# Performance work log

Hardware: AMD Instinct MI355X
Metric: run time of the kernel (lower is better)

## Reference

```python
import jax, jax.numpy as jnp
import numpy as np
from jax.ops import segment_sum

N = 100000
E = 3200000
IN_DIM = 256
OUT_DIM = 64
LN_EPS = 1e-5
NEG_SLOPE = 0.01


def setup_inputs() -> dict:
    key = jax.random.key(0)
    k1, k2, k3, k4, k5 = jax.random.split(key, 5)
    x = jax.random.normal(k1, (N, IN_DIM), dtype=jnp.float32)
    edge_index = jax.random.randint(k2, (2, E), 0, N, dtype=jnp.int32)
    edge_weight = jax.random.uniform(k3, (E,), dtype=jnp.float32)
    # GCNConv params (glorot-ish scale) + LayerNorm params
    W = jax.random.normal(k4, (IN_DIM, OUT_DIM), dtype=jnp.float32) / np.sqrt(IN_DIM)
    b = jnp.zeros((OUT_DIM,), dtype=jnp.float32)
    gamma = jnp.ones((OUT_DIM,), dtype=jnp.float32)
    beta = jnp.zeros((OUT_DIM,), dtype=jnp.float32)
    return {"x": x, "edge_index": edge_index, "edge_weight": edge_weight,
            "W": W, "b": b, "gamma": gamma, "beta": beta}


def _gcn_forward(x, edge_index, edge_weight, W, b, gamma, beta):
    n = x.shape[0]
    # add self-loops with weight 1 (PyG GCNConv default)
    loops = jnp.arange(n, dtype=edge_index.dtype)
    src = jnp.concatenate([edge_index[0], loops])   # [E+N] message sources
    dst = jnp.concatenate([edge_index[1], loops])   # [E+N] aggregation targets
    ew = jnp.concatenate([edge_weight, jnp.ones((n,), dtype=edge_weight.dtype)])
    # symmetric normalization: deg computed on dst via weighted scatter
    deg = segment_sum(ew, dst, num_segments=n)                   # [N]
    dinv = jnp.where(deg > 0, jax.lax.rsqrt(deg), 0.0)           # deg^{-1/2}
    norm = dinv[src] * ew * dinv[dst]                            # [E+N]
    h = x @ W                                                    # [N, OUT]
    agg = segment_sum(h[src] * norm[:, None], dst, num_segments=n)  # [N, OUT]
    y = agg + b
    # leaky_relu then LayerNorm over last dim
    y = jnp.where(y >= 0, y, NEG_SLOPE * y)
    mu = jnp.mean(y, axis=-1, keepdims=True)
    var = jnp.mean(jnp.square(y - mu), axis=-1, keepdims=True)
    return (y - mu) * jax.lax.rsqrt(var + LN_EPS) * gamma + beta


def reference(x, edge_index, edge_weight, W, b, gamma, beta):
    return _gcn_forward(x, edge_index, edge_weight, W, b, gamma, beta)
```

## Files before the change

### kernel.cpp

```cpp
#include <hip/hip_runtime.h>

#define NN 100000
#define NE 3200000
#define OVCAP 65536

#define BINSZ 64
#define NBIN ((NN + BINSZ - 1) / BINSZ)
#define MAXPB 4096
#define SCAT_BLOCKS 512

struct OvEnt { int dst; int src; float ew; int pad; };


__global__ void k_zero(int* __restrict__ bincnt, int* __restrict__ ovcnt, int n) {
    int i = blockIdx.x * 256 + threadIdx.x;
    if (i < n) bincnt[i] = 0;
    if (i == 0) *ovcnt = 0;
}

__global__ __launch_bounds__(256) void k_binscatter(
    const int* __restrict__ src, const int* __restrict__ dst,
    const float* __restrict__ ew, int* __restrict__ bincnt,
    uint2* __restrict__ binbuf, int cap,
    OvEnt* __restrict__ ov, int* __restrict__ ovcnt, int e) {
    __shared__ int hist[NBIN];
    int t = threadIdx.x;
    int chunk = (e + gridDim.x - 1) / gridDim.x;
    int beg = blockIdx.x * chunk;
    int end = beg + chunk; if (end > e) end = e;
    for (int j = t; j < NBIN; j += 256) hist[j] = 0;
    __syncthreads();
    for (int i = beg + t; i < end; i += 256)
        atomicAdd(&hist[dst[i] >> 6], 1);
    __syncthreads();
    for (int j = t; j < NBIN; j += 256) {
        int c = hist[j];
        hist[j] = (c > 0) ? atomicAdd(&bincnt[j], c) : 0;
    }
    __syncthreads();
    for (int i = beg + t; i < end; i += 256) {
        int s = src[i], d = dst[i];
        float w = ew[i];
        int bin = d >> 6;
        int pos = atomicAdd(&hist[bin], 1);
        if (pos < cap) {
            unsigned key = (unsigned)s | ((unsigned)(d & 63) << 17);
            binbuf[(size_t)bin * cap + pos] = make_uint2(key, __float_as_uint(w));
        } else {
            int op = atomicAdd(ovcnt, 1);
            if (op < OVCAP) { OvEnt t2; t2.dst = d; t2.src = s; t2.ew = w; t2.pad = 0; ov[op] = t2; }
        }
    }
}

__global__ __launch_bounds__(256) void k_deg2(
    const int* __restrict__ bincnt, const uint2* __restrict__ binbuf, int cap,
    const OvEnt* __restrict__ ov, const int* __restrict__ ovcnt,
    float* __restrict__ dinv, int n) {
    __shared__ float sdeg[BINSZ];
    int bin = blockIdx.x, t = threadIdx.x;
    if (t < BINSZ) sdeg[t] = 0.f;
    __syncthreads();
    int cnt = bincnt[bin];
    int bc = cnt < cap ? cnt : cap;
    const uint2* base = binbuf + (size_t)bin * cap;
    for (int i = t; i < bc; i += 256) {
        uint2 v = base[i];
        atomicAdd(&sdeg[(v.x >> 17) & 63u], __uint_as_float(v.y));
    }
    if (cnt > cap) {
        int on = *ovcnt; if (on > OVCAP) on = OVCAP;
        for (int j = t; j < on; j += 256) {
            OvEnt e2 = ov[j];
            if ((e2.dst >> 6) == bin) atomicAdd(&sdeg[e2.dst & 63], e2.ew);
        }
    }
    __syncthreads();
    if (t < BINSZ) {
        int g = bin * BINSZ + t;
        if (g < n) dinv[g] = rsqrtf(1.0f + sdeg[t]);
    }
}

__global__ __launch_bounds__(512) void k_sortgather(
    const float* __restrict__ h, const float* __restrict__ dinv,
    const int* __restrict__ bincnt, const uint2* __restrict__ binbuf, int cap,
    const OvEnt* __restrict__ ov, const int* __restrict__ ovcnt,
    const float* __restrict__ bias, const float* __restrict__ gamma,
    const float* __restrict__ beta, float* __restrict__ out, int n) {
    __shared__ uint2 sbuf[MAXPB];
    __shared__ float sd[BINSZ];
    __shared__ int hcnt[BINSZ];
    __shared__ int hoff[BINSZ];
    __shared__ int noff[BINSZ];
    int bin = blockIdx.x, t = threadIdx.x;
    int lane = t & 63, wid = t >> 6;

    if (t < BINSZ) {
        hcnt[t] = 0;
        int g = bin * BINSZ + t;
        sd[t] = (g < n) ? dinv[g] : 0.f;
    }
    __syncthreads();
    int cnt = bincnt[bin];
    int bc = cnt < cap ? cnt : cap;
    const uint2* base = binbuf + (size_t)bin * cap;

    uint2 ent[8];
    int ne = 0;
#pragma unroll
    for (int p = 0; p < 8; p++) {
        int idx = t + p * 512;
        if (idx < bc) { ent[p] = base[idx]; ne = p + 1; }
    }
#pragma unroll
    for (int p = 0; p < 8; p++)
        if (p < ne) atomicAdd(&hcnt[(int)((ent[p].x >> 17) & 63u)], 1);
    __syncthreads();
    if (t < 64) {
        int v = hcnt[t], inc = v;
#pragma unroll
        for (int o2 = 1; o2 < 64; o2 <<= 1) {
            int u = __shfl_up(inc, o2, 64);
            if (t >= o2) inc += u;
        }
        int excl = inc - v;
        hoff[t] = excl;
        noff[t] = excl;
    }
    __syncthreads();
#pragma unroll
    for (int p = 0; p < 8; p++) {
        if (p < ne) {
            int dl = (int)((ent[p].x >> 17) & 63u);
            int pos = atomicAdd(&hoff[dl], 1);
            sbuf[pos] = ent[p];
        }
    }
    __syncthreads();

    int sov = (cnt > cap);
    float bi = bias[lane], ga = gamma[lane], be = beta[lane];
    for (int dl = wid; dl < BINSZ; dl += 8) {
        int g = bin * BINSZ + dl;
        if (g >= n) break;
        float di = sd[dl];
        float acc = h[(size_t)g * 64 + lane] * di * di;
        int start = noff[dl], c0 = hcnt[dl];
        for (int j = 0; j < c0; j += 64) {
            int c = c0 - j; if (c > 64) c = 64;
            int s = 0; float w = 0.f;
            if (lane < c) {
                uint2 v = sbuf[start + j + lane];
                s = (int)(v.x & 0x1FFFFu);
                w = __uint_as_float(v.y) * dinv[s] * di;
            }
            int i2 = 0;
            for (; i2 + 16 <= c; i2 += 16) {
                float hv[16], wv[16];
#pragma unroll
                for (int q = 0; q < 16; q++) {
                    int si = __shfl(s, i2 + q, 64);
                    wv[q] = __shfl(w, i2 + q, 64);
                    hv[q] = h[(size_t)si * 64 + lane];
                }
#pragma unroll
                for (int q = 0; q < 16; q++) acc += hv[q] * wv[q];
            }
            if (i2 < c) {
                float hv[16], wv[16];
                int rem = c - i2;
#pragma unroll
                for (int q = 0; q < 16; q++) {
                    if (q < rem) {
                        int si = __shfl(s, i2 + q, 64);
                        wv[q] = __shfl(w, i2 + q, 64);
                        hv[q] = h[(size_t)si * 64 + lane];
                    } else { wv[q] = 0.f; hv[q] = 0.f; }
                }
#pragma unroll
                for (int q = 0; q < 16; q++) acc += hv[q] * wv[q];
            }
        }
        if (sov) {
            int on = *ovcnt; if (on > OVCAP) on = OVCAP;
            for (int j2 = 0; j2 < on; j2++) {
                OvEnt e2 = ov[j2];
                if (e2.dst == g)
                    acc += h[(size_t)e2.src * 64 + lane] * dinv[e2.src] * e2.ew * di;
            }
        }
        float y = acc + bi;
        y = (y >= 0.f) ? y : 0.01f * y;
        float sum = y;
#pragma unroll
        for (int o = 32; o > 0; o >>= 1) sum += __shfl_xor(sum, o, 64);
        float mu = sum * (1.0f / 64.0f);
        float d = y - mu;
        float v = d * d;
#pragma unroll
        for (int o = 32; o > 0; o >>= 1) v += __shfl_xor(v, o, 64);
        v *= (1.0f / 64.0f);
        out[(size_t)g * 64 + lane] = d * rsqrtf(v + 1e-5f) * ga + be;
    }
}

#define GR 64
#define GKC 32
#define XS_STRIDE 36
__global__ __launch_bounds__(256) void k_gemm(const float* __restrict__ x,
                                              const float* __restrict__ W,
                                              float* __restrict__ h, int n) {
    __shared__ float xs[GR][XS_STRIDE];
    __shared__ float wsh[GKC][64];
    int t = threadIdx.x;
    int tx = t & 15;
    int ty = t >> 4;
    int rbase = blockIdx.x * GR;
    float acc[4][4];
#pragma unroll
    for (int i = 0; i < 4; i++)
#pragma unroll
        for (int j = 0; j < 4; j++) acc[i][j] = 0.0f;

    for (int k0 = 0; k0 < 256; k0 += GKC) {
        const float4* wsrc = (const float4*)(W + k0 * 64);
        float4* wdst = (float4*)(&wsh[0][0]);
        wdst[t] = wsrc[t];
        wdst[t + 256] = wsrc[t + 256];
#pragma unroll
        for (int p = 0; p < 2; p++) {
            int f4 = p * 256 + t;
            int r = f4 >> 3;
            int kq = (f4 & 7) << 2;
            int row = rbase + r;
            float4 val = make_float4(0.f, 0.f, 0.f, 0.f);
            if (row < n) val = *(const float4*)(x + (size_t)row * 256 + k0 + kq);
            *(float4*)(&xs[r][kq]) = val;
        }
        __syncthreads();
        int r0 = ty * 4, c0 = tx * 4;
#pragma unroll
        for (int kk = 0; kk < GKC; kk += 4) {
            float4 wv[4];
#pragma unroll
            for (int m = 0; m < 4; m++) wv[m] = *(const float4*)(&wsh[kk + m][c0]);
#pragma unroll
            for (int i = 0; i < 4; i++) {
                float4 xv = *(const float4*)(&xs[r0 + i][kk]);
                acc[i][0] += xv.x * wv[0].x + xv.y * wv[1].x + xv.z * wv[2].x + xv.w * wv[3].x;
                acc[i][1] += xv.x * wv[0].y + xv.y * wv[1].y + xv.z * wv[2].y + xv.w * wv[3].y;
                acc[i][2] += xv.x * wv[0].z + xv.y * wv[1].z + xv.z * wv[2].z + xv.w * wv[3].z;
                acc[i][3] += xv.x * wv[0].w + xv.y * wv[1].w + xv.z * wv[2].w + xv.w * wv[3].w;
            }
        }
        __syncthreads();
    }
    int r0 = ty * 4, c0 = tx * 4;
#pragma unroll
    for (int i = 0; i < 4; i++) {
        int row = rbase + r0 + i;
        if (row < n) {
            float4 v = make_float4(acc[i][0], acc[i][1], acc[i][2], acc[i][3]);
            *(float4*)(h + (size_t)row * 64 + c0) = v;
        }
    }
}


__global__ void k_init(float* __restrict__ deg, int* __restrict__ cnt, int n) {
    int i = blockIdx.x * 256 + threadIdx.x;
    if (i < n) { deg[i] = 1.0f; cnt[i] = 0; }
}

__global__ void k_deg(const int* __restrict__ dst, const float* __restrict__ ew,
                      float* __restrict__ deg, int* __restrict__ cnt, int e) {
    int i = blockIdx.x * 256 + threadIdx.x;
    if (i < e) {
        int d = dst[i];
        atomicAdd(&deg[d], ew[i]);
        atomicAdd(&cnt[d], 1);
    }
}

#define SCAN_T 256
#define SCAN_E 8
__global__ void k_scan_blocks(const int* __restrict__ cnt, int* __restrict__ off,
                              int* __restrict__ bsum, int n) {
    __shared__ int sdata[SCAN_T];
    int base = blockIdx.x * (SCAN_T * SCAN_E);
    int t = threadIdx.x;
    int v[SCAN_E];
    int local = 0;
    int idx0 = base + t * SCAN_E;
#pragma unroll
    for (int i = 0; i < SCAN_E; i++) {
        int idx = idx0 + i;
        int c = (idx < n) ? cnt[idx] : 0;
        v[i] = local;
        local += c;
    }
    sdata[t] = local;
    __syncthreads();
    for (int o = 1; o < SCAN_T; o <<= 1) {
        int x = 0;
        if (t >= o) x = sdata[t - o];
        __syncthreads();
        sdata[t] += x;
        __syncthreads();
    }
    int excl = sdata[t] - local;
#pragma unroll
    for (int i = 0; i < SCAN_E; i++) {
        int idx = idx0 + i;
        if (idx < n) off[idx] = excl + v[i];
    }
    if (t == SCAN_T - 1) bsum[blockIdx.x] = sdata[t];
}

__global__ void k_scan_bsums(int* __restrict__ bsum, int nb) {
    int t = threadIdx.x;
    int v = (t < nb) ? bsum[t] : 0;
    int orig = v;
#pragma unroll
    for (int o = 1; o < 64; o <<= 1) {
        int u = __shfl_up(v, o, 64);
        if (t >= o) v += u;
    }
    if (t < nb) bsum[t] = v - orig;
}

__global__ void k_finalize(int* __restrict__ off, const int* __restrict__ bsum,
                           int* __restrict__ cursor, float* __restrict__ deg,
                           int n, int total) {
    int i = blockIdx.x * 256 + threadIdx.x;
    if (i < n) {
        int o = off[i] + bsum[i >> 11];
        off[i] = o;
        cursor[i] = o;
        deg[i] = rsqrtf(deg[i]);
    }
    if (i == 0) off[n] = total;
}

__global__ void k_scatter(const int* __restrict__ src, const int* __restrict__ dst,
                          const float* __restrict__ ew, const float* __restrict__ dinv,
                          int* __restrict__ cursor, int* __restrict__ ssrc,
                          float* __restrict__ snorm, int e) {
    int i = blockIdx.x * 256 + threadIdx.x;
    if (i < e) {
        int s = src[i], d = dst[i];
        float nm = dinv[s] * ew[i] * dinv[d];
        int pos = atomicAdd(&cursor[d], 1);
        ssrc[pos] = s;
        snorm[pos] = nm;
    }
}

__global__ __launch_bounds__(256) void k_gather(
    const float* __restrict__ h, const float* __restrict__ dinv,
    const int* __restrict__ off, const int* __restrict__ ssrc,
    const float* __restrict__ snorm, const float* __restrict__ bias,
    const float* __restrict__ gamma, const float* __restrict__ beta,
    float* __restrict__ out, int n) {
    int lane = threadIdx.x & 63;
    int wid = threadIdx.x >> 6;
    int node = blockIdx.x * 4 + wid;
    if (node >= n) return;
    float di = dinv[node];
    float acc = h[(size_t)node * 64 + lane] * di * di;
    int beg = off[node], end = off[node + 1];
    for (int j = beg; j < end; j += 64) {
        int cnt = end - j;
        if (cnt > 64) cnt = 64;
        int s = 0;
        float w = 0.f;
        if (lane < cnt) { s = ssrc[j + lane]; w = snorm[j + lane]; }
        for (int i2 = 0; i2 < cnt; i2++) {
            int si = __shfl(s, i2, 64);
            float wi = __shfl(w, i2, 64);
            acc += h[(size_t)si * 64 + lane] * wi;
        }
    }
    float y = acc + bias[lane];
    y = (y >= 0.f) ? y : 0.01f * y;
    float sum = y;
#pragma unroll
    for (int o = 32; o > 0; o >>= 1) sum += __shfl_xor(sum, o, 64);
    float mu = sum * (1.0f / 64.0f);
    float d = y - mu;
    float v = d * d;
#pragma unroll
    for (int o = 32; o > 0; o >>= 1) v += __shfl_xor(v, o, 64);
    v *= (1.0f / 64.0f);
    out[(size_t)node * 64 + lane] = d * rsqrtf(v + 1e-5f) * gamma[lane] + beta[lane];
}


extern "C" void kernel_launch(void* const* d_in, const int* in_sizes, int n_in,
                              void* d_out, int out_size, void* d_ws, size_t ws_size,
                              hipStream_t stream) {
    const float* x = (const float*)d_in[0];
    const int* ei = (const int*)d_in[1];
    const float* ew = (const float*)d_in[2];
    const float* W = (const float*)d_in[3];
    const float* b = (const float*)d_in[4];
    const float* gamma = (const float*)d_in[5];
    const float* beta = (const float*)d_in[6];
    float* out = (float*)d_out;

    const int n = NN, e = NE;
    const int* src = ei;
    const int* dst = ei + e;

    char* ws = (char*)d_ws;
    size_t o = 0;
    auto alloc = [&](size_t bytes) -> char* {
        char* r = ws + o;
        o = (o + bytes + 255) & ~(size_t)255;
        return r;
    };
    auto pad = [](size_t bytes) -> size_t { return (bytes + 255) & ~(size_t)255; };

    int nb_n = (n + 255) / 256;
    int nb_e = (e + 255) / 256;
    int nb_gemm = (n + GR - 1) / GR;

    size_t fixed = 0;
    fixed += pad((size_t)NBIN * 4);
    fixed += 256;
    fixed += pad((size_t)OVCAP * 16);
    fixed += pad((size_t)n * 4);
    fixed += pad((size_t)n * 64 * 4);

    int cap = 0;
    if (ws_size >= fixed + pad((size_t)NBIN * 4096 * 8) + 8192) cap = 4096;
    else if (ws_size >= fixed + pad((size_t)NBIN * 3072 * 8) + 8192) cap = 3072;

    if (cap > 0) {
        int* bincnt = (int*)alloc((size_t)NBIN * 4);
        int* ovcnt = (int*)alloc(4);
        OvEnt* ov = (OvEnt*)alloc((size_t)OVCAP * 16);
        float* dinv = (float*)alloc((size_t)n * 4);
        float* h = (float*)alloc((size_t)n * 64 * 4);
        uint2* binbuf = (uint2*)alloc((size_t)NBIN * cap * 8);

        int nb_z = (NBIN + 255) / 256;
        k_zero<<<nb_z, 256, 0, stream>>>(bincnt, ovcnt, NBIN);
        k_binscatter<<<SCAT_BLOCKS, 256, 0, stream>>>(src, dst, ew, bincnt, binbuf, cap,
                                                      ov, ovcnt, e);
        k_deg2<<<NBIN, 256, 0, stream>>>(bincnt, binbuf, cap, ov, ovcnt, dinv, n);
        k_gemm<<<nb_gemm, 256, 0, stream>>>(x, W, h, n);
        k_sortgather<<<NBIN, 512, 0, stream>>>(h, dinv, bincnt, binbuf, cap,
                                               ov, ovcnt, b, gamma, beta, out, n);
    } else {
        float* deg = (float*)alloc((size_t)n * 4);
        int* cnt = (int*)alloc((size_t)n * 4);
        int* off = (int*)alloc((size_t)(n + 1) * 4);
        int* cursor = (int*)alloc((size_t)n * 4);
        int* bsum = (int*)alloc(64 * 4);
        float* h = (float*)alloc((size_t)n * 64 * 4);
        int* ssrc = (int*)alloc((size_t)e * 4);
        float* snorm = (float*)alloc((size_t)e * 4);
        int nb_scan = (n + SCAN_T * SCAN_E - 1) / (SCAN_T * SCAN_E);
        int nb_w = (n + 3) / 4;

        k_init<<<nb_n, 256, 0, stream>>>(deg, cnt, n);
        k_deg<<<nb_e, 256, 0, stream>>>(dst, ew, deg, cnt, e);
        k_scan_blocks<<<nb_scan, SCAN_T, 0, stream>>>(cnt, off, bsum, n);
        k_scan_bsums<<<1, 64, 0, stream>>>(bsum, nb_scan);
        k_finalize<<<nb_n, 256, 0, stream>>>(off, bsum, cursor, deg, n, e);
        k_scatter<<<nb_e, 256, 0, stream>>>(src, dst, ew, deg, cursor, ssrc, snorm, e);
        k_gemm<<<nb_gemm, 256, 0, stream>>>(x, W, h, n);
        k_gather<<<nb_w, 256, 0, stream>>>(h, deg, off, ssrc, snorm, b, gamma, beta, out, n);
    }
}
```

Before: 472.0 us.

## Merge GEMM and edge bin-scatter into one launch running concurrently

Combines the binned edge scatter kernel and the dense x@W GEMM into a single kernel whose first SCAT_BLOCKS blocks do the scatter and whose remaining blocks compute h. The two independent phases (one atomic and latency-bound, one bandwidth and compute-bound) can then share the GPU at the same time, and one launch is removed. Both paths share a 17 KB shared-memory buffer, which may reduce occupancy for the scatter blocks.

```diff
diff --git a/kernel.cpp b/kernel.cpp
--- a/kernel.cpp
+++ b/kernel.cpp
@@ -9,6 +9,10 @@
 #define MAXPB 4096
 #define SCAT_BLOCKS 512
 
+#define GR 64
+#define GKC 32
+#define XS_STRIDE 36
+
 struct OvEnt { int dst; int src; float ew; int pad; };
 
 
@@ -18,37 +22,97 @@
     if (i == 0) *ovcnt = 0;
 }
 
-__global__ __launch_bounds__(256) void k_binscatter(
+__global__ __launch_bounds__(256) void k_gemm_scatter(
+    const float* __restrict__ x, const float* __restrict__ W,
+    float* __restrict__ h,
     const int* __restrict__ src, const int* __restrict__ dst,
     const float* __restrict__ ew, int* __restrict__ bincnt,
     uint2* __restrict__ binbuf, int cap,
-    OvEnt* __restrict__ ov, int* __restrict__ ovcnt, int e) {
-    __shared__ int hist[NBIN];
+    OvEnt* __restrict__ ov, int* __restrict__ ovcnt, int e, int n) {
+    __shared__ char smem[17408];
     int t = threadIdx.x;
-    int chunk = (e + gridDim.x - 1) / gridDim.x;
-    int beg = blockIdx.x * chunk;
-    int end = beg + chunk; if (end > e) end = e;
-    for (int j = t; j < NBIN; j += 256) hist[j] = 0;
-    __syncthreads();
-    for (int i = beg + t; i < end; i += 256)
-        atomicAdd(&hist[dst[i] >> 6], 1);
-    __syncthreads();
-    for (int j = t; j < NBIN; j += 256) {
-        int c = hist[j];
-        hist[j] = (c > 0) ? atomicAdd(&bincnt[j], c) : 0;
-    }
-    __syncthreads();
-    for (int i = beg + t; i < end; i += 256) {
-        int s = src[i], d = dst[i];
-        float w = ew[i];
-        int bin = d >> 6;
-        int pos = atomicAdd(&hist[bin], 1);
-        if (pos < cap) {
-            unsigned key = (unsigned)s | ((unsigned)(d & 63) << 17);
-            binbuf[(size_t)bin * cap + pos] = make_uint2(key, __float_as_uint(w));
-        } else {
-            int op = atomicAdd(ovcnt, 1);
-            if (op < OVCAP) { OvEnt t2; t2.dst = d; t2.src = s; t2.ew = w; t2.pad = 0; ov[op] = t2; }
+
+    if (blockIdx.x < SCAT_BLOCKS) {
+        int* hist = (int*)smem;
+        int chunk = (e + SCAT_BLOCKS - 1) / SCAT_BLOCKS;
+        int beg = blockIdx.x * chunk;
+        int end = beg + chunk; if (end > e) end = e;
+        for (int j = t; j < NBIN; j += 256) hist[j] = 0;
+        __syncthreads();
+        for (int i = beg + t; i < end; i += 256)
+            atomicAdd(&hist[dst[i] >> 6], 1);
+        __syncthreads();
+        for (int j = t; j < NBIN; j += 256) {
+            int c = hist[j];
+            hist[j] = (c > 0) ? atomicAdd(&bincnt[j], c) : 0;
+        }
+        __syncthreads();
+        for (int i = beg + t; i < end; i += 256) {
+            int s = src[i], d = dst[i];
+            float w = ew[i];
+            int bin = d >> 6;
+            int pos = atomicAdd(&hist[bin], 1);
+            if (pos < cap) {
+                unsigned key = (unsigned)s | ((unsigned)(d & 63) << 17);
+                binbuf[(size_t)bin * cap + pos] = make_uint2(key, __float_as_uint(w));
+            } else {
+                int op = atomicAdd(ovcnt, 1);
+                if (op < OVCAP) { OvEnt t2; t2.dst = d; t2.src = s; t2.ew = w; t2.pad = 0; ov[op] = t2; }
+            }
+        }
+    } else {
+        float (*xs)[XS_STRIDE] = (float(*)[XS_STRIDE])smem;
+        float (*wsh)[64] = (float(*)[64])(smem + 9216);
+        int tx = t & 15;
+        int ty = t >> 4;
+        int rbase = (blockIdx.x - SCAT_BLOCKS) * GR;
+        float acc[4][4];
+#pragma unroll
+        for (int i = 0; i < 4; i++)
+#pragma unroll
+            for (int j = 0; j < 4; j++) acc[i][j] = 0.0f;
+
+        for (int k0 = 0; k0 < 256; k0 += GKC) {
+            const float4* wsrc = (const float4*)(W + k0 * 64);
+            float4* wdst = (float4*)(&wsh[0][0]);
+            wdst[t] = wsrc[t];
+            wdst[t + 256] = wsrc[t + 256];
+#pragma unroll
+            for (int p = 0; p < 2; p++) {
+                int f4 = p * 256 + t;
+                int r = f4 >> 3;
+                int kq = (f4 & 7) << 2;
+                int row = rbase + r;
+                float4 val = make_float4(0.f, 0.f, 0.f, 0.f);
+                if (row < n) val = *(const float4*)(x + (size_t)row * 256 + k0 + kq);
+                *(float4*)(&xs[r][kq]) = val;
+            }
+            __syncthreads();
+            int r0 = ty * 4, c0 = tx * 4;
+#pragma unroll
+            for (int kk = 0; kk < GKC; kk += 4) {
+                float4 wv[4];
+#pragma unroll
+                for (int m = 0; m < 4; m++) wv[m] = *(const float4*)(&wsh[kk + m][c0]);
+#pragma unroll
+                for (int i = 0; i < 4; i++) {
+                    float4 xv = *(const float4*)(&xs[r0 + i][kk]);
+                    acc[i][0] += xv.x * wv[0].x + xv.y * wv[1].x + xv.z * wv[2].x + xv.w * wv[3].x;
+                    acc[i][1] += xv.x * wv[0].y + xv.y * wv[1].y + xv.z * wv[2].y + xv.w * wv[3].y;
+                    acc[i][2] += xv.x * wv[0].z + xv.y * wv[1].z + xv.z * wv[2].z + xv.w * wv[3].z;
+                    acc[i][3] += xv.x * wv[0].w + xv.y * wv[1].w + xv.z * wv[2].w + xv.w * wv[3].w;
+                }
+            }
+            __syncthreads();
+        }
+        int r0 = ty * 4, c0 = tx * 4;
+#pragma unroll
+        for (int i = 0; i < 4; i++) {
+            int row = rbase + r0 + i;
+            if (row < n) {
+                float4 v = make_float4(acc[i][0], acc[i][1], acc[i][2], acc[i][3]);
+                *(float4*)(h + (size_t)row * 64 + c0) = v;
+            }
         }
     }
 }
@@ -205,9 +269,6 @@
     }
 }
 
-#define GR 64
-#define GKC 32
-#define XS_STRIDE 36
 __global__ __launch_bounds__(256) void k_gemm(const float* __restrict__ x,
                                               const float* __restrict__ W,
                                               float* __restrict__ h, int n) {
@@ -447,10 +508,9 @@
 
         int nb_z = (NBIN + 255) / 256;
         k_zero<<<nb_z, 256, 0, stream>>>(bincnt, ovcnt, NBIN);
-        k_binscatter<<<SCAT_BLOCKS, 256, 0, stream>>>(src, dst, ew, bincnt, binbuf, cap,
-                                                      ov, ovcnt, e);
+        k_gemm_scatter<<<SCAT_BLOCKS + nb_gemm, 256, 0, stream>>>(
+            x, W, h, src, dst, ew, bincnt, binbuf, cap, ov, ovcnt, e, n);
         k_deg2<<<NBIN, 256, 0, stream>>>(bincnt, binbuf, cap, ov, ovcnt, dinv, n);
-        k_gemm<<<nb_gemm, 256, 0, stream>>>(x, W, h, n);
         k_sortgather<<<NBIN, 512, 0, stream>>>(h, dinv, bincnt, binbuf, cap,
                                                ov, ovcnt, b, gamma, beta, out, n);
     } else {
```

New measurement: 457.0 us. 3.2% less time.
